# Kernel tuning notes

Measured on AMD Instinct MI355X. Metric: run time of the kernel, lower is better.

Reference implementation:

```python
import jax, jax.numpy as jnp
import numpy as np

NODE_DIM = 32
NUM_NODES = 256
BATCH = 32
HIDDEN = 64


def setup_inputs() -> dict:
    key = jax.random.key(0)
    k1, k2, k3, k4, k5 = jax.random.split(key, 5)
    node_features = jax.random.normal(k1, (BATCH, NUM_NODES, NODE_DIM), dtype=jnp.float32)
    # nn.Linear(node_dim*2, 64): weight [64, 2*node_dim], bias [64]
    s1 = 1.0 / np.sqrt(2 * NODE_DIM)
    W1 = jax.random.uniform(k2, (HIDDEN, 2 * NODE_DIM), minval=-s1, maxval=s1, dtype=jnp.float32)
    b1 = jax.random.uniform(k3, (HIDDEN,), minval=-s1, maxval=s1, dtype=jnp.float32)
    # nn.Linear(64, 1): weight [1, 64], bias [1]
    s2 = 1.0 / np.sqrt(HIDDEN)
    W2 = jax.random.uniform(k4, (1, HIDDEN), minval=-s2, maxval=s2, dtype=jnp.float32)
    b2 = jax.random.uniform(k5, (1,), minval=-s2, maxval=s2, dtype=jnp.float32)
    return {"node_features": node_features, "W1": W1, "b1": b1, "W2": W2, "b2": b2}


def reference(node_features, W1, b1, W2, b2):
    # fc1(concat(x_i, x_j)) splits as x_i @ W1a^T + x_j @ W1b^T (exact same math,
    # avoids materializing the [B,N,N,2d] pair tensor).
    d = node_features.shape[-1]
    W1a, W1b = W1[:, :d], W1[:, d:]
    Ai = jnp.einsum('bnd,hd->bnh', node_features, W1a)  # [B,N,H]
    Aj = jnp.einsum('bnd,hd->bnh', node_features, W1b)  # [B,N,H]
    hidden = jax.nn.relu(Ai[:, :, None, :] + Aj[:, None, :, :] + b1)  # [B,N,N,H]
    logits = jnp.einsum('bijh,h->bij', hidden, W2[0]) + b2[0]  # [B,N,N]
    return jax.nn.sigmoid(logits)
```

## Files before the change

### kernel.cpp

```cpp
#include <hip/hip_runtime.h>

typedef _Float16 h2 __attribute__((ext_vector_type(2)));
typedef _Float16 h8 __attribute__((ext_vector_type(8)));

#define BB 32
#define NN 256
#define DD 32
#define HH 64
#define ETI 128
#define ETJ 64
#define XST 40
#define AST 72

#if defined(__has_builtin)
#  if __has_builtin(__builtin_amdgcn_fdot2)
#    define FDOT2(a, b, c) __builtin_amdgcn_fdot2((a), (b), (c), false)
#  endif
#endif
#ifndef FDOT2
#  define FDOT2(a, b, c) ((c) + (float)((a)[0]) * (float)((b)[0]) + (float)((a)[1]) * (float)((b)[1]))
#endif

__device__ __forceinline__ float sigmoidf_fast(float v) {
    return 1.0f / (1.0f + __expf(-v));
}

__global__ __launch_bounds__(512) void fused_kernel(const float* __restrict__ x, const float* __restrict__ W1,
                                                    const float* __restrict__ b1, const float* __restrict__ W2,
                                                    const float* __restrict__ b2, float* __restrict__ out)
{
    __shared__ _Float16 sX[192][XST];
    __shared__ _Float16 sW[128][XST];
    __shared__ _Float16 sAi[ETI][AST];
    __shared__ _Float16 sAj[ETJ][AST];
    __shared__ _Float16 sW2h[HH];
    __shared__ float sb1[HH];

    const int blk = blockIdx.x;
    const int jt = blk & 3;
    const int it = (blk >> 2) & 1;
    const int b  = blk >> 3;
    const int tid = threadIdx.x;
    const float* xb = x + (size_t)b * NN * DD;

    {
        const int hc = tid >> 2, d0 = (tid & 3) << 3;
        const float* src = (hc < HH) ? &W1[hc * 64 + d0] : &W1[(hc - HH) * 64 + DD + d0];
        float t8[8];
        *(float4*)&t8[0] = *(const float4*)&src[0];
        *(float4*)&t8[4] = *(const float4*)&src[4];
        const int phys = (hc >> 3) + ((hc & 7) << 4);
        h8 v;
#pragma unroll
        for (int q = 0; q < 8; ++q) v[q] = (_Float16)t8[q];
        *(h8*)&sW[phys][d0] = v;
    }
    if (tid < 384) {
        const int row = tid >> 1, d0 = (tid & 1) << 4;
        int grow, phys;
        if (row < 128) { grow = it * ETI + row; phys = (row >> 2) + ((row & 3) << 5); }
        else { const int r = row - 128; grow = jt * ETJ + r; phys = 128 + (r >> 1) + ((r & 1) << 5); }
        float t16[16];
        const float* src = &xb[(size_t)grow * DD + d0];
        *(float4*)&t16[0]  = *(const float4*)&src[0];
        *(float4*)&t16[4]  = *(const float4*)&src[4];
        *(float4*)&t16[8]  = *(const float4*)&src[8];
        *(float4*)&t16[12] = *(const float4*)&src[12];
        h8 v0, v1;
#pragma unroll
        for (int q = 0; q < 8; ++q) { v0[q] = (_Float16)t16[q]; v1[q] = (_Float16)t16[q + 8]; }
        *(h8*)&sX[phys][d0]     = v0;
        *(h8*)&sX[phys][d0 + 8] = v1;
    }
    if (tid < HH) sW2h[tid] = (_Float16)W2[tid];
    else if (tid < 2 * HH) sb1[tid - HH] = b1[tid - HH];
    __syncthreads();

    {
        const int wid = tid >> 6, lane = tid & 63;
        const int lq = lane >> 3, lp = lane & 7;
        if (wid < 4) {
            const int g = (wid << 3) | lq;
            float pacc[4][8] = {};
#pragma unroll
            for (int ch = 0; ch < 4; ++ch) {
                h8 xv[4], wv[8];
#pragma unroll
                for (int rr = 0; rr < 4; ++rr) xv[rr] = *(const h8*)&sX[g + (rr << 5)][ch << 3];
#pragma unroll
                for (int cc = 0; cc < 8; ++cc) wv[cc] = *(const h8*)&sW[lp + (cc << 4)][ch << 3];
#pragma unroll
                for (int rr = 0; rr < 4; ++rr)
#pragma unroll
                    for (int cc = 0; cc < 8; ++cc) {
                        float a = pacc[rr][cc];
                        a = FDOT2(__builtin_shufflevector(xv[rr], xv[rr], 0, 1), __builtin_shufflevector(wv[cc], wv[cc], 0, 1), a);
                        a = FDOT2(__builtin_shufflevector(xv[rr], xv[rr], 2, 3), __builtin_shufflevector(wv[cc], wv[cc], 2, 3), a);
                        a = FDOT2(__builtin_shufflevector(xv[rr], xv[rr], 4, 5), __builtin_shufflevector(wv[cc], wv[cc], 4, 5), a);
                        a = FDOT2(__builtin_shufflevector(xv[rr], xv[rr], 6, 7), __builtin_shufflevector(wv[cc], wv[cc], 6, 7), a);
                        pacc[rr][cc] = a;
                    }
            }
#pragma unroll
            for (int rr = 0; rr < 4; ++rr) {
                h8 v;
#pragma unroll
                for (int cc = 0; cc < 8; ++cc) v[cc] = (_Float16)pacc[rr][cc];
                *(h8*)&sAi[(g << 2) | rr][lp << 3] = v;
            }
        } else {
            const int g = ((wid - 4) << 3) | lq;
            float pacc[2][8] = {};
#pragma unroll
            for (int ch = 0; ch < 4; ++ch) {
                h8 xv[2], wv[8];
#pragma unroll
                for (int rr = 0; rr < 2; ++rr) xv[rr] = *(const h8*)&sX[128 + g + (rr << 5)][ch << 3];
#pragma unroll
                for (int cc = 0; cc < 8; ++cc) wv[cc] = *(const h8*)&sW[8 + lp + (cc << 4)][ch << 3];
#pragma unroll
                for (int rr = 0; rr < 2; ++rr)
#pragma unroll
                    for (int cc = 0; cc < 8; ++cc) {
                        float a = pacc[rr][cc];
                        a = FDOT2(__builtin_shufflevector(xv[rr], xv[rr], 0, 1), __builtin_shufflevector(wv[cc], wv[cc], 0, 1), a);
                        a = FDOT2(__builtin_shufflevector(xv[rr], xv[rr], 2, 3), __builtin_shufflevector(wv[cc], wv[cc], 2, 3), a);
                        a = FDOT2(__builtin_shufflevector(xv[rr], xv[rr], 4, 5), __builtin_shufflevector(wv[cc], wv[cc], 4, 5), a);
                        a = FDOT2(__builtin_shufflevector(xv[rr], xv[rr], 6, 7), __builtin_shufflevector(wv[cc], wv[cc], 6, 7), a);
                        pacc[rr][cc] = a;
                    }
            }
#pragma unroll
            for (int rr = 0; rr < 2; ++rr) {
                h8 v;
#pragma unroll
                for (int cc = 0; cc < 8; ++cc) v[cc] = (_Float16)(pacc[rr][cc] + sb1[(lp << 3) + cc]);
                *(h8*)&sAj[(g << 1) | rr][lp << 3] = v;
            }
        }
    }
    __syncthreads();

    const int jl = tid & 15;
    const int il = tid >> 4;
    h8 w2v[8];
#pragma unroll
    for (int q = 0; q < 8; ++q) w2v[q] = *(const h8*)&sW2h[q << 3];

    float eacc[4][4] = {};
#pragma unroll
    for (int c8 = 0; c8 < 8; ++c8) {
        h8 av[4], cv[4];
#pragma unroll
        for (int r = 0; r < 4; ++r) av[r] = *(const h8*)&sAi[il + (r << 5)][c8 << 3];
#pragma unroll
        for (int c = 0; c < 4; ++c) cv[c] = *(const h8*)&sAj[jl + (c << 4)][c8 << 3];
#pragma unroll
        for (int r = 0; r < 4; ++r)
#pragma unroll
            for (int c = 0; c < 4; ++c) {
                h8 z  = av[r] + cv[c];
                h8 rl = __builtin_elementwise_max(z, h8{});
                float a = eacc[r][c];
                a = FDOT2(__builtin_shufflevector(rl, rl, 0, 1), __builtin_shufflevector(w2v[c8], w2v[c8], 0, 1), a);
                a = FDOT2(__builtin_shufflevector(rl, rl, 2, 3), __builtin_shufflevector(w2v[c8], w2v[c8], 2, 3), a);
                a = FDOT2(__builtin_shufflevector(rl, rl, 4, 5), __builtin_shufflevector(w2v[c8], w2v[c8], 4, 5), a);
                a = FDOT2(__builtin_shufflevector(rl, rl, 6, 7), __builtin_shufflevector(w2v[c8], w2v[c8], 6, 7), a);
                eacc[r][c] = a;
            }
    }

    const float b2v = b2[0];
    const size_t base = (((size_t)(b * NN) + it * ETI + il) << 8) + jt * ETJ + jl;
#pragma unroll
    for (int r = 0; r < 4; ++r)
#pragma unroll
        for (int c = 0; c < 4; ++c)
            out[base + (size_t)(r << 5) * NN + (c << 4)] = sigmoidf_fast(eacc[r][c] + b2v);
}

extern "C" void kernel_launch(void* const* d_in, const int* in_sizes, int n_in,
                              void* d_out, int out_size, void* d_ws, size_t ws_size,
                              hipStream_t stream) {
    const float* x  = (const float*)d_in[0];
    const float* W1 = (const float*)d_in[1];
    const float* b1 = (const float*)d_in[2];
    const float* W2 = (const float*)d_in[3];
    const float* b2 = (const float*)d_in[4];
    float* out = (float*)d_out;

    const int nBlocks = BB * (NN / ETI) * (NN / ETJ);
    fused_kernel<<<nBlocks, 512, 0, stream>>>(x, W1, b1, W2, b2, out);
}
```

Measured before the change: 16.98 us.

## Remap j-columns per thread for float4 stores and consolidate projection waves

Changes the X/Aj shared-memory row permutation so each thread owns four consecutive output columns, which lets the epilogue write float4 stores instead of strided scalar stores. The projection phase is reorganized so only three waves (two for Ai, one for Aj) compute 8x8 register tiles, with the other waves idle during that phase. The b2 bias is folded into the accumulator initialization, and launch bounds request two blocks per CU. This trades a less balanced projection phase and higher register pressure for wider coalesced global writes.

Measured after the change: 17.60 us. +3.7%, slower.

```diff
diff --git a/kernel.cpp b/kernel.cpp
--- a/kernel.cpp
+++ b/kernel.cpp
@@ -1,14 +1,11 @@
 #include <hip/hip_runtime.h>
 
-typedef _Float16 h2 __attribute__((ext_vector_type(2)));
 typedef _Float16 h8 __attribute__((ext_vector_type(8)));
 
 #define BB 32
 #define NN 256
 #define DD 32
 #define HH 64
-#define ETI 128
-#define ETJ 64
 #define XST 40
 #define AST 72
 
@@ -25,14 +22,14 @@
     return 1.0f / (1.0f + __expf(-v));
 }
 
-__global__ __launch_bounds__(512) void fused_kernel(const float* __restrict__ x, const float* __restrict__ W1,
-                                                    const float* __restrict__ b1, const float* __restrict__ W2,
-                                                    const float* __restrict__ b2, float* __restrict__ out)
+__global__ __launch_bounds__(512, 2) void fused_kernel(const float* __restrict__ x, const float* __restrict__ W1,
+                                                       const float* __restrict__ b1, const float* __restrict__ W2,
+                                                       const float* __restrict__ b2, float* __restrict__ out)
 {
     __shared__ _Float16 sX[192][XST];
     __shared__ _Float16 sW[128][XST];
-    __shared__ _Float16 sAi[ETI][AST];
-    __shared__ _Float16 sAj[ETJ][AST];
+    __shared__ _Float16 sAi[128][AST];
+    __shared__ _Float16 sAj[64][AST];
     __shared__ _Float16 sW2h[HH];
     __shared__ float sb1[HH];
 
@@ -58,8 +55,8 @@
     if (tid < 384) {
         const int row = tid >> 1, d0 = (tid & 1) << 4;
         int grow, phys;
-        if (row < 128) { grow = it * ETI + row; phys = (row >> 2) + ((row & 3) << 5); }
-        else { const int r = row - 128; grow = jt * ETJ + r; phys = 128 + (r >> 1) + ((r & 1) << 5); }
+        if (row < 128) { grow = it * 128 + row; phys = (row >> 3) + ((row & 7) << 4); }
+        else { const int r = row - 128; grow = jt * 64 + r; phys = 128 + (r >> 3) + ((r & 7) << 3); }
         float t16[16];
         const float* src = &xb[(size_t)grow * DD + d0];
         *(float4*)&t16[0]  = *(const float4*)&src[0];
@@ -78,19 +75,18 @@
 
     {
         const int wid = tid >> 6, lane = tid & 63;
-        const int lq = lane >> 3, lp = lane & 7;
-        if (wid < 4) {
-            const int g = (wid << 3) | lq;
-            float pacc[4][8] = {};
+        if (wid < 2) {
+            const int rg = (wid << 3) | (lane >> 3), hg = lane & 7;
+            float pacc[8][8] = {};
 #pragma unroll
             for (int ch = 0; ch < 4; ++ch) {
-                h8 xv[4], wv[8];
+                h8 xv[8], wv[8];
 #pragma unroll
-                for (int rr = 0; rr < 4; ++rr) xv[rr] = *(const h8*)&sX[g + (rr << 5)][ch << 3];
+                for (int rr = 0; rr < 8; ++rr) xv[rr] = *(const h8*)&sX[rg + (rr << 4)][ch << 3];
 #pragma unroll
-                for (int cc = 0; cc < 8; ++cc) wv[cc] = *(const h8*)&sW[lp + (cc << 4)][ch << 3];
+                for (int cc = 0; cc < 8; ++cc) wv[cc] = *(const h8*)&sW[hg + (cc << 4)][ch << 3];
 #pragma unroll
-                for (int rr = 0; rr < 4; ++rr)
+                for (int rr = 0; rr < 8; ++rr)
 #pragma unroll
                     for (int cc = 0; cc < 8; ++cc) {
                         float a = pacc[rr][cc];
@@ -102,24 +98,24 @@
                     }
             }
 #pragma unroll
-            for (int rr = 0; rr < 4; ++rr) {
+            for (int rr = 0; rr < 8; ++rr) {
                 h8 v;
 #pragma unroll
                 for (int cc = 0; cc < 8; ++cc) v[cc] = (_Float16)pacc[rr][cc];
-                *(h8*)&sAi[(g << 2) | rr][lp << 3] = v;
+                *(h8*)&sAi[(rg << 3) | rr][hg << 3] = v;
             }
-        } else {
-            const int g = ((wid - 4) << 3) | lq;
-            float pacc[2][8] = {};
+        } else if (wid == 2) {
+            const int lq = lane >> 3, lp = lane & 7;
+            float pacc[8][8] = {};
 #pragma unroll
             for (int ch = 0; ch < 4; ++ch) {
-                h8 xv[2], wv[8];
+                h8 xv[8], wv[8];
 #pragma unroll
-                for (int rr = 0; rr < 2; ++rr) xv[rr] = *(const h8*)&sX[128 + g + (rr << 5)][ch << 3];
+                for (int rr = 0; rr < 8; ++rr) xv[rr] = *(const h8*)&sX[128 + lq + (rr << 3)][ch << 3];
 #pragma unroll
                 for (int cc = 0; cc < 8; ++cc) wv[cc] = *(const h8*)&sW[8 + lp + (cc << 4)][ch << 3];
 #pragma unroll
-                for (int rr = 0; rr < 2; ++rr)
+                for (int rr = 0; rr < 8; ++rr)
 #pragma unroll
                     for (int cc = 0; cc < 8; ++cc) {
                         float a = pacc[rr][cc];
@@ -131,11 +127,11 @@
                     }
             }
 #pragma unroll
-            for (int rr = 0; rr < 2; ++rr) {
+            for (int rr = 0; rr < 8; ++rr) {
                 h8 v;
 #pragma unroll
                 for (int cc = 0; cc < 8; ++cc) v[cc] = (_Float16)(pacc[rr][cc] + sb1[(lp << 3) + cc]);
-                *(h8*)&sAj[(g << 1) | rr][lp << 3] = v;
+                *(h8*)&sAj[(lq << 1) + (rr >> 2) + ((rr & 3) << 4)][lp << 3] = v;
             }
         }
     }
@@ -147,7 +143,13 @@
 #pragma unroll
     for (int q = 0; q < 8; ++q) w2v[q] = *(const h8*)&sW2h[q << 3];
 
-    float eacc[4][4] = {};
+    const float b2v = b2[0];
+    float eacc[4][4];
+#pragma unroll
+    for (int r = 0; r < 4; ++r)
+#pragma unroll
+        for (int c = 0; c < 4; ++c) eacc[r][c] = b2v;
+
 #pragma unroll
     for (int c8 = 0; c8 < 8; ++c8) {
         h8 av[4], cv[4];
@@ -170,13 +172,15 @@
             }
     }
 
-    const float b2v = b2[0];
-    const size_t base = (((size_t)(b * NN) + it * ETI + il) << 8) + jt * ETJ + jl;
 #pragma unroll
-    for (int r = 0; r < 4; ++r)
-#pragma unroll
-        for (int c = 0; c < 4; ++c)
-            out[base + (size_t)(r << 5) * NN + (c << 4)] = sigmoidf_fast(eacc[r][c] + b2v);
+    for (int r = 0; r < 4; ++r) {
+        float4 o;
+        o.x = sigmoidf_fast(eacc[r][0]);
+        o.y = sigmoidf_fast(eacc[r][1]);
+        o.z = sigmoidf_fast(eacc[r][2]);
+        o.w = sigmoidf_fast(eacc[r][3]);
+        *(float4*)&out[((size_t)(b * NN) + it * 128 + il + (r << 5)) * NN + jt * 64 + (jl << 2)] = o;
+    }
 }
 
 extern "C" void kernel_launch(void* const* d_in, const int* in_sizes, int n_in,
@@ -189,6 +193,6 @@
     const float* b2 = (const float*)d_in[4];
     float* out = (float*)d_out;
 
-    const int nBlocks = BB * (NN / ETI) * (NN / ETJ);
+    const int nBlocks = BB * (NN / 128) * (NN / 64);
     fused_kernel<<<nBlocks, 512, 0, stream>>>(x, W1, b1, W2, b2, out);
 }
```
